# Optimization experiments

Measured on AMD Instinct MI355X. Metric: run time of the kernel, lower is better.

Reference implementation:

```python
import jax, jax.numpy as jnp
import numpy as np

N_HEAD = 12

def setup_inputs() -> dict:
    key = jax.random.key(0)
    k1, k2, k3 = jax.random.split(key, 3)
    B, T, C = 4, 2048, 768
    x = jax.random.normal(k1, (B, T, C), dtype=jnp.float32)
    # c_attn params (Linear(n_embd, 3*n_embd)); stored as [in, out] for x @ W
    W_attn = jax.random.normal(k2, (C, 3 * C), dtype=jnp.float32) * (1.0 / np.sqrt(C))
    b_attn = jax.random.normal(k3, (3 * C,), dtype=jnp.float32) * 0.02
    return {"x": x, "W_attn": W_attn, "b_attn": b_attn}

def reference(x, W_attn, b_attn):
    B, T, C = x.shape
    H = N_HEAD
    Dh = C // H
    qkv = x @ W_attn + b_attn                      # [B,T,3C]
    q, k, v = jnp.split(qkv, 3, axis=-1)
    q = q.reshape(B, T, H, Dh)
    k = k.reshape(B, T, H, Dh)
    v = v.reshape(B, T, H, Dh)
    scale = 1.0 / np.sqrt(Dh)
    # scaled QK^T per head: [B,H,T,T]
    scores = jnp.einsum('bqhd,bkhd->bhqk', q * scale, k)
    causal = jnp.tril(jnp.ones((T, T), dtype=bool))  # [T,T]
    # masked-to--inf then ReLU == zero out non-causal and clamp at 0
    p = jnp.where(causal, jnp.maximum(scores, 0.0), 0.0)
    y = jnp.einsum('bhqk,bkhd->bqhd', p, v).reshape(B, T, C)
    return y
```

## Files before the change

### kernel.cpp

```cpp
#include <hip/hip_runtime.h>
#include <cstdint>
#include <cstddef>

typedef unsigned short u16;
typedef unsigned int u32;
typedef __bf16 bf16x8 __attribute__((ext_vector_type(8)));
typedef float f32x4 __attribute__((ext_vector_type(4)));

__device__ __forceinline__ u16 f2bf(float f) {
    unsigned int x = __builtin_bit_cast(unsigned int, f);
    x += 0x7FFFu + ((x >> 16) & 1u);
    return (u16)(x >> 16);
}

__device__ __forceinline__ bf16x8 ldfrag(const u16* p) {
    bf16x8 r;
    __builtin_memcpy(&r, (const u16*)__builtin_assume_aligned(p, 16), 16);
    return r;
}

__device__ __forceinline__ int4 ldg16(const u16* p) {
    int4 r;
    __builtin_memcpy(&r, (const u16*)__builtin_assume_aligned(p, 16), 16);
    return r;
}

__device__ __forceinline__ void async16(u16* lds, const u16* g) {
    __builtin_amdgcn_global_load_lds(
        (const __attribute__((address_space(1))) void*)g,
        (__attribute__((address_space(3))) void*)lds,
        16, 0, 0);
}

__global__ __launch_bounds__(256) void cvt_bf16(const float* __restrict__ in,
                                                u16* __restrict__ out, int n) {
    int i = (blockIdx.x * 256 + threadIdx.x) * 4;
    if (i >= n) return;
    float4 v = *reinterpret_cast<const float4*>(in + i);
    union { u16 e[4]; unsigned long long u; } w;
    w.e[0] = f2bf(v.x); w.e[1] = f2bf(v.y); w.e[2] = f2bf(v.z); w.e[3] = f2bf(v.w);
    *reinterpret_cast<unsigned long long*>(out + i) = w.u;
}

__global__ __launch_bounds__(256) void wt_transpose(const float* __restrict__ W,
                                                    u16* __restrict__ Wt) {
    const int R = 768, Ccols = 2304;
    __shared__ float tile[32][33];
    const int bx = blockIdx.x * 32;
    const int by = blockIdx.y * 32;
    const int tx = threadIdx.x & 31, ty = threadIdx.x >> 5;
    #pragma unroll
    for (int i = 0; i < 32; i += 8)
        tile[ty + i][tx] = W[(size_t)(by + ty + i) * Ccols + bx + tx];
    __syncthreads();
    #pragma unroll
    for (int i = 0; i < 32; i += 8)
        Wt[(size_t)(bx + ty + i) * R + by + tx] = f2bf(tile[tx][ty + i]);
}

__global__ __launch_bounds__(256) void qkv_gemm(const u16* __restrict__ A,
                                                const u16* __restrict__ Bt,
                                                const float* __restrict__ bias,
                                                u16* __restrict__ C) {
    const int N = 2304, K = 768;
    __shared__ __align__(16) u16 sA[128 * 64];
    __shared__ __align__(16) u16 sB[128 * 64];
    const int t = threadIdx.x;
    const int wave = t >> 6, lane = t & 63;
    const int quad = lane >> 4, l16 = lane & 15;
    const int wr = wave >> 1, wc = wave & 1;
    const int m0 = blockIdx.y * 128, n0 = blockIdx.x * 128;

    const int srow_base = wave * 8 + (lane >> 3);
    const int schunk = lane & 7;
    const int swz = (lane >> 3) & 7;

    f32x4 acc[4][4] = {};

    for (int k0 = 0; k0 < K; k0 += 64) {
        __syncthreads();
        #pragma unroll
        for (int j = 0; j < 4; ++j) {
            const int row = j * 32 + srow_base;
            const int dch = schunk ^ swz;
            async16(sA + j * 2048 + wave * 512, A + (size_t)(m0 + row) * K + k0 + dch * 8);
            async16(sB + j * 2048 + wave * 512, Bt + (size_t)(n0 + row) * K + k0 + dch * 8);
        }
        __syncthreads();

        bf16x8 af[4][2], bfr[4][2];
        const int rsw = l16 & 7;
        #pragma unroll
        for (int i = 0; i < 4; ++i)
            #pragma unroll
            for (int h = 0; h < 2; ++h) {
                af[i][h] = ldfrag(sA + (wr * 64 + i * 16 + l16) * 64 + (((h * 4 + quad) ^ rsw) << 3));
                bfr[i][h] = ldfrag(sB + (wc * 64 + i * 16 + l16) * 64 + (((h * 4 + quad) ^ rsw) << 3));
            }
        #pragma unroll
        for (int h = 0; h < 2; ++h)
            #pragma unroll
            for (int i = 0; i < 4; ++i)
                #pragma unroll
                for (int j = 0; j < 4; ++j)
                    acc[i][j] = __builtin_amdgcn_mfma_f32_16x16x32_bf16(af[i][h], bfr[j][h], acc[i][j], 0, 0, 0);
    }

    #pragma unroll
    for (int i = 0; i < 4; ++i)
        #pragma unroll
        for (int j = 0; j < 4; ++j) {
            const int col = n0 + wc * 64 + j * 16 + l16;
            const float bc = bias[col];
            const float scale = (col < 768) ? 0.125f : 1.0f;
            #pragma unroll
            for (int r = 0; r < 4; ++r) {
                const int row = m0 + wr * 64 + i * 16 + quad * 4 + r;
                C[(size_t)row * N + col] = f2bf((acc[i][j][r] + bc) * scale);
            }
        }
}

__global__ __launch_bounds__(256, 3) void attn_kernel(const u16* __restrict__ qkv,
                                                      float* __restrict__ out) {
    const int T = 2048, C3 = 2304, Cc = 768, Dh = 64;

    const int bid = blockIdx.x;
    const int rr = bid >> 8;
    const int ss = bid & 255;
    const int x = ss & 15;
    const int qa = (rr == 0) ? x : (rr == 1) ? (15 - x) : ((x + 8) & 15);
    const int qb = 31 - qa;
    const int hb = (ss >> 4) + (rr << 4);
    const int h = hb % 12, b = hb / 12;

    const int t = threadIdx.x;
    const int wave = t >> 6, lane = t & 63;
    const int quad = lane >> 4, l16 = lane & 15;

    __shared__ __align__(16) u16 sK[2][64 * 64];
    __shared__ __align__(16) u32 sVt[2][64 * 36];
    __shared__ __align__(16) u16 sP[128 * 72];

    const u16* qbase = qkv + (size_t)b * T * C3 + (size_t)h * Dh;
    const u16* kbase = qbase + Cc;
    const u16* vbase = qbase + 2 * Cc;

    bf16x8 qf[8][2];
    #pragma unroll
    for (int cg = 0; cg < 8; ++cg) {
        const int qrow = ((cg < 4) ? qa * 64 : (qb * 64 - 64)) + cg * 16 + l16;
        const u16* p = qbase + (size_t)qrow * C3 + quad * 8;
        qf[cg][0] = ldfrag(p);
        qf[cg][1] = ldfrag(p + 32);
    }

    f32x4 oacc[2][4] = {};

    const int tp = t & 31, dg = t >> 5;
    const int krow_b = wave * 8 + (lane >> 3);
    const int kswz = (lane >> 3) & 7;
    const int kch = (lane & 7) ^ kswz;

    int4 v0r, v1r;
    auto loadV = [&](int it) {
        const u16* vp = vbase + (size_t)(it * 64 + 2 * tp) * C3 + dg * 8;
        v0r = ldg16(vp);
        v1r = ldg16(vp + C3);
    };
    auto stageK = [&](int it, int bi) {
        #pragma unroll
        for (int j = 0; j < 2; ++j)
            async16(&sK[bi][0] + j * 2048 + wave * 512,
                    kbase + (size_t)(it * 64 + j * 32 + krow_b) * C3 + kch * 8);
    };
    auto writeV = [&](int bi) {
        union { int4 v; u16 e[8]; } ua, ub;
        ua.v = v0r; ub.v = v1r;
        #pragma unroll
        for (int i = 0; i < 8; ++i)
            sVt[bi][(dg * 8 + i) * 36 + tp] = (u32)ua.e[i] | ((u32)ub.e[i] << 16);
    };

    loadV(0);
    stageK(0, 0);
    writeV(0);
    __syncthreads();

    int buf = 0;
    for (int it = 0; it <= qb; ++it) {
        const bool more = (it < qb);
        if (more) { loadV(it + 1); stageK(it + 1, buf ^ 1); }

        const bool act_a = (it <= qa);

        bf16x8 kf0, kf1;
        {
            const u16* kr = &sK[buf][0] + (wave * 16 + l16) * 64;
            const int rsw = l16 & 7;
            kf0 = ldfrag(kr + ((quad ^ rsw) << 3));
            kf1 = ldfrag(kr + (((quad + 4) ^ rsw) << 3));
        }
        const int cg_lo = act_a ? 0 : 4;
        #pragma unroll
        for (int cg = 7; cg >= 0; --cg) {
            if (cg < cg_lo) break;
            f32x4 s = {};
            s = __builtin_amdgcn_mfma_f32_16x16x32_bf16(kf0, qf[cg][0], s, 0, 0, 0);
            s = __builtin_amdgcn_mfma_f32_16x16x32_bf16(kf1, qf[cg][1], s, 0, 0, 0);
            const bool diag = (cg < 4) ? (it == qa) : (it == qb);
            u32 bits[4];
            #pragma unroll
            for (int r = 0; r < 4; ++r) {
                float v = fmaxf(s[r], 0.0f);
                if (diag && (wave * 16 + quad * 4 + r > (cg & 3) * 16 + l16)) v = 0.0f;
                bits[r] = __builtin_bit_cast(u32, v);
            }
            u32 pk[2];
            pk[0] = (bits[1] & 0xFFFF0000u) | (bits[0] >> 16);
            pk[1] = (bits[3] & 0xFFFF0000u) | (bits[2] >> 16);
            __builtin_memcpy((u16*)__builtin_assume_aligned(
                                 sP + (cg * 16 + l16) * 72 + wave * 16 + quad * 4, 8),
                             pk, 8);
        }

        asm volatile("s_waitcnt lgkmcnt(0)" ::: "memory");
        __builtin_amdgcn_s_barrier();
        asm volatile("" ::: "memory");

        const u16* sVb = (const u16*)sVt[buf];
        #pragma unroll
        for (int kk = 0; kk < 2; ++kk) {
            bf16x8 ap1 = ldfrag(sP + (64 + wave * 16 + l16) * 72 + kk * 32 + quad * 8);
            bf16x8 ap0;
            if (act_a) ap0 = ldfrag(sP + (wave * 16 + l16) * 72 + kk * 32 + quad * 8);
            #pragma unroll
            for (int dt = 0; dt < 4; ++dt) {
                bf16x8 bv = ldfrag(sVb + (dt * 16 + l16) * 72 + kk * 32 + quad * 8);
                oacc[1][dt] = __builtin_amdgcn_mfma_f32_16x16x32_bf16(ap1, bv, oacc[1][dt], 0, 0, 0);
                if (act_a)
                    oacc[0][dt] = __builtin_amdgcn_mfma_f32_16x16x32_bf16(ap0, bv, oacc[0][dt], 0, 0, 0);
            }
        }

        if (more) writeV(buf ^ 1);
        __syncthreads();
        buf ^= 1;
    }

    #pragma unroll
    for (int g = 0; g < 2; ++g)
        #pragma unroll
        for (int dt = 0; dt < 4; ++dt)
            #pragma unroll
            for (int r = 0; r < 4; ++r) {
                const int tok = (g == 0 ? qa * 64 : qb * 64) + wave * 16 + quad * 4 + r;
                const int c = h * Dh + dt * 16 + l16;
                out[((size_t)b * T + tok) * Cc + c] = oacc[g][dt][r];
            }
}

extern "C" void kernel_launch(void* const* d_in, const int* in_sizes, int n_in,
                              void* d_out, int out_size, void* d_ws, size_t ws_size,
                              hipStream_t stream) {
    const float* x    = (const float*)d_in[0];
    const float* W    = (const float*)d_in[1];
    const float* bias = (const float*)d_in[2];
    float* out = (float*)d_out;

    char* ws = (char*)d_ws;
    const size_t xb_bytes = (size_t)8192 * 768 * 2;
    const size_t wt_bytes = (size_t)2304 * 768 * 2;
    u16* xb  = (u16*)ws;
    u16* Wt  = (u16*)(ws + xb_bytes);
    u16* qkv = (u16*)(ws + xb_bytes + wt_bytes);

    cvt_bf16<<<6144, 256, 0, stream>>>(x, xb, 8192 * 768);
    wt_transpose<<<dim3(72, 24), 256, 0, stream>>>(W, Wt);
    qkv_gemm<<<dim3(18, 64), 256, 0, stream>>>(xb, Wt, bias, qkv);
    attn_kernel<<<768, 256, 0, stream>>>(qkv, out);
}
```

Before: 187.4 us.

## Load K fragments directly from global into registers, add MFMA priority hints

The K tile is no longer staged through double-buffered shared memory with async copies. Each lane now loads its own K fragments straight from global memory into registers, prefetching one iteration ahead. The change also wraps the MFMA sections in s_setprio raises and replaces __syncthreads with an explicit lgkmcnt wait plus barrier. This frees LDS and removes the LDS reads for K. In exchange it adds register pressure and makes uncoalesced per-lane global loads whose latency must be hidden, and the end-of-loop barrier no longer waits on vmcnt.

```diff
diff --git a/kernel.cpp b/kernel.cpp
--- a/kernel.cpp
+++ b/kernel.cpp
@@ -138,7 +138,6 @@
     const int wave = t >> 6, lane = t & 63;
     const int quad = lane >> 4, l16 = lane & 15;
 
-    __shared__ __align__(16) u16 sK[2][64 * 64];
     __shared__ __align__(16) u32 sVt[2][64 * 36];
     __shared__ __align__(16) u16 sP[128 * 72];
 
@@ -158,9 +157,6 @@
     f32x4 oacc[2][4] = {};
 
     const int tp = t & 31, dg = t >> 5;
-    const int krow_b = wave * 8 + (lane >> 3);
-    const int kswz = (lane >> 3) & 7;
-    const int kch = (lane & 7) ^ kswz;
 
     int4 v0r, v1r;
     auto loadV = [&](int it) {
@@ -168,11 +164,10 @@
         v0r = ldg16(vp);
         v1r = ldg16(vp + C3);
     };
-    auto stageK = [&](int it, int bi) {
-        #pragma unroll
-        for (int j = 0; j < 2; ++j)
-            async16(&sK[bi][0] + j * 2048 + wave * 512,
-                    kbase + (size_t)(it * 64 + j * 32 + krow_b) * C3 + kch * 8);
+    auto ldgK = [&](int it, bf16x8& f0, bf16x8& f1) {
+        const u16* kp = kbase + (size_t)(it * 64 + wave * 16 + l16) * C3 + quad * 8;
+        f0 = ldfrag(kp);
+        f1 = ldfrag(kp + 32);
     };
     auto writeV = [&](int bi) {
         union { int4 v; u16 e[8]; } ua, ub;
@@ -182,32 +177,27 @@
             sVt[bi][(dg * 8 + i) * 36 + tp] = (u32)ua.e[i] | ((u32)ub.e[i] << 16);
     };
 
+    bf16x8 kc0, kc1, kn0, kn1;
     loadV(0);
-    stageK(0, 0);
+    ldgK(0, kc0, kc1);
     writeV(0);
     __syncthreads();
 
     int buf = 0;
     for (int it = 0; it <= qb; ++it) {
         const bool more = (it < qb);
-        if (more) { loadV(it + 1); stageK(it + 1, buf ^ 1); }
+        if (more) { loadV(it + 1); ldgK(it + 1, kn0, kn1); }
 
         const bool act_a = (it <= qa);
 
-        bf16x8 kf0, kf1;
-        {
-            const u16* kr = &sK[buf][0] + (wave * 16 + l16) * 64;
-            const int rsw = l16 & 7;
-            kf0 = ldfrag(kr + ((quad ^ rsw) << 3));
-            kf1 = ldfrag(kr + (((quad + 4) ^ rsw) << 3));
-        }
         const int cg_lo = act_a ? 0 : 4;
+        __builtin_amdgcn_s_setprio(1);
         #pragma unroll
         for (int cg = 7; cg >= 0; --cg) {
             if (cg < cg_lo) break;
             f32x4 s = {};
-            s = __builtin_amdgcn_mfma_f32_16x16x32_bf16(kf0, qf[cg][0], s, 0, 0, 0);
-            s = __builtin_amdgcn_mfma_f32_16x16x32_bf16(kf1, qf[cg][1], s, 0, 0, 0);
+            s = __builtin_amdgcn_mfma_f32_16x16x32_bf16(kc0, qf[cg][0], s, 0, 0, 0);
+            s = __builtin_amdgcn_mfma_f32_16x16x32_bf16(kc1, qf[cg][1], s, 0, 0, 0);
             const bool diag = (cg < 4) ? (it == qa) : (it == qb);
             u32 bits[4];
             #pragma unroll
@@ -223,12 +213,14 @@
                                  sP + (cg * 16 + l16) * 72 + wave * 16 + quad * 4, 8),
                              pk, 8);
         }
+        __builtin_amdgcn_s_setprio(0);
 
         asm volatile("s_waitcnt lgkmcnt(0)" ::: "memory");
         __builtin_amdgcn_s_barrier();
         asm volatile("" ::: "memory");
 
         const u16* sVb = (const u16*)sVt[buf];
+        __builtin_amdgcn_s_setprio(1);
         #pragma unroll
         for (int kk = 0; kk < 2; ++kk) {
             bf16x8 ap1 = ldfrag(sP + (64 + wave * 16 + l16) * 72 + kk * 32 + quad * 8);
@@ -242,9 +234,15 @@
                     oacc[0][dt] = __builtin_amdgcn_mfma_f32_16x16x32_bf16(ap0, bv, oacc[0][dt], 0, 0, 0);
             }
         }
+        __builtin_amdgcn_s_setprio(0);
 
         if (more) writeV(buf ^ 1);
-        __syncthreads();
+
+        asm volatile("s_waitcnt lgkmcnt(0)" ::: "memory");
+        __builtin_amdgcn_s_barrier();
+        asm volatile("" ::: "memory");
+
+        kc0 = kn0; kc1 = kn1;
         buf ^= 1;
     }
 
```

After: 183.4 us. 1.02x faster.
